# Optimization experiments

Hardware: AMD Instinct MI355X
Metric: run time of the kernel (lower is better)

The kernel has to match this reference:

```python
import jax, jax.numpy as jnp
import numpy as np

B, S, D, H = 2, 2048, 1024, 16
HD = D // H                      # 64
NUM_ROPE_DIMS = 2
NF = HD // (2 * NUM_ROPE_DIMS)   # 16 freqs per rope dim -> total HD//2
FFN_H = 4 * D


def householder_matrix(vs):
    """Product of Householder reflections: Q = prod_i (I - 2 v_i v_i^T / ||v_i||^2)."""
    dim = vs.shape[-1]
    def step(Q, v):
        v = v[:, None]
        Q = Q - (2.0 / (jnp.sum(v * v) + 1e-8)) * (v @ (v.T @ Q))
        return Q, None
    Q, _ = jax.lax.scan(step, jnp.eye(dim, dtype=vs.dtype), vs)
    return Q


def rmsnorm(x):
    # torch.nn.RMSNorm(eps=None) uses dtype eps, no affine
    return x * jax.lax.rsqrt(jnp.mean(x * x, axis=-1, keepdims=True) + jnp.finfo(x.dtype).eps)


def setup_inputs() -> dict:
    key = jax.random.key(0)
    ks = jax.random.split(key, 8)
    x = jax.random.normal(ks[0], (B, S, D), jnp.float32)
    mask = jnp.tril(jnp.ones((S, S), dtype=bool))          # causal block mask
    qkv_w = jax.random.normal(ks[1], (3 * D, D), jnp.float32) * 0.02
    out_w = jax.random.normal(ks[2], (D, D), jnp.float32) * 0.02
    gate_w = jax.random.normal(ks[3], (D, D), jnp.float32) * 0.02
    gate_b = jnp.zeros((D,), jnp.float32)
    w12 = jax.random.normal(ks[4], (2 * FFN_H, D), jnp.float32) * 0.02
    w3 = jax.random.normal(ks[5], (D, FFN_H), jnp.float32) * 0.02
    hh_vs = jax.random.normal(ks[6], (HD // 2, HD), jnp.float32) * 0.02
    inv_freq = 1.0 / (10000.0 ** (jnp.arange(NF, dtype=jnp.float32) / NF))
    pos = jnp.arange(S, dtype=jnp.float32)
    rope_pos = jnp.stack([pos, pos], axis=-1)              # [S, num_rope_dims]
    return dict(x=x, mask=mask, qkv_w=qkv_w, out_w=out_w, gate_w=gate_w,
                gate_b=gate_b, w12=w12, w3=w3, hh_vs=hh_vs,
                inv_freq=inv_freq, rope_pos=rope_pos)


def reference(x, mask, qkv_w, out_w, gate_w, gate_b, w12, w3, hh_vs, inv_freq, rope_pos):
    Bs, Ss, Ds = x.shape
    resid = x
    xn = rmsnorm(x)
    qkv = xn @ qkv_w.T                                      # [B,S,3D]
    q, k, v = jnp.split(qkv, 3, axis=-1)
    q = q.reshape(Bs, Ss, H, HD).transpose(0, 2, 1, 3)      # [B,H,S,HD]
    k = k.reshape(Bs, Ss, H, HD).transpose(0, 2, 1, 3)
    v = v.reshape(Bs, Ss, H, HD).transpose(0, 2, 1, 3)

    # RnRoPE: rotate into canonical basis, apply RoPE, rotate back
    Q = householder_matrix(hh_vs)                           # [HD,HD]
    q = q @ Q.T
    k = k @ Q.T
    # geo_state.scale = 1.0
    full = jnp.einsum('sd,f->sdf', rope_pos, inv_freq).reshape(Ss, -1)  # [S, HD//2]
    half = HD // 2
    full = full[:, :half]
    emb = jnp.concatenate([full, full], axis=-1)            # [S, HD]
    cos, sin = jnp.cos(emb), jnp.sin(emb)

    def rot(t):
        t1, t2 = jnp.split(t, 2, axis=-1)
        return t * cos + jnp.concatenate([-t2, t1], axis=-1) * sin

    q = rot(q) @ Q
    k = rot(k) @ Q

    # block-masked attention (flex_attention default scale = 1/sqrt(HD))
    scores = jnp.einsum('bhsd,bhtd->bhst', q, k) / jnp.sqrt(jnp.asarray(HD, x.dtype))
    scores = jnp.where(mask, scores, -jnp.inf)
    attn = jax.nn.softmax(scores, axis=-1)
    o = jnp.einsum('bhst,bhtd->bhsd', attn, v)
    o = o.transpose(0, 2, 1, 3).reshape(Bs, Ss, Ds)
    o = o @ out_w.T
    gate = jax.nn.sigmoid(o @ gate_w.T + gate_b)
    x = resid + o * gate

    # SwiGLU FFN
    resid2 = x
    xn2 = rmsnorm(x)
    x12 = xn2 @ w12.T
    x1, x2 = jnp.split(x12, 2, axis=-1)
    ffn = (jax.nn.silu(x1) * x2) @ w3.T
    return resid2 + ffn
```

## Files before the change

kernel.cpp:

```cpp
#include <hip/hip_runtime.h>
#include <hip/hip_bf16.h>
#include <math.h>

constexpr int Bc = 2, Sc = 2048, Dc = 1024, Hc = 16, HDc = 64;
constexpr int D3 = 3 * Dc;

typedef __bf16 bf16x8 __attribute__((ext_vector_type(8)));
typedef float f32x4 __attribute__((ext_vector_type(4)));

__device__ __forceinline__ void gll16(const void* g, void* l) {
  __builtin_amdgcn_global_load_lds((const __attribute__((address_space(1))) unsigned int*)g,
                                   (__attribute__((address_space(3))) unsigned int*)l,
                                   16, 0, 0);
}

__device__ __forceinline__ unsigned short f2bf(float v) {
  __hip_bfloat16 h = __float2bfloat16(v);
  return *(unsigned short*)&h;
}
__device__ __forceinline__ float b2f(unsigned short u) {
  unsigned v = ((unsigned)u) << 16;
  return __uint_as_float(v);
}

#define SBAR() asm volatile("s_barrier" ::: "memory")

__global__ __launch_bounds__(256) void f2b_kernel(const float* __restrict__ in,
                                                  unsigned short* __restrict__ out) {
  int i = blockIdx.x * 256 + threadIdx.x;
  float4 v = ((const float4*)in)[i];
  ushort4 o;
  o.x = f2bf(v.x); o.y = f2bf(v.y); o.z = f2bf(v.z); o.w = f2bf(v.w);
  ((ushort4*)out)[i] = o;
}

__global__ __launch_bounds__(256) void w12i_kernel(const float* __restrict__ in,
                                                   unsigned short* __restrict__ out) {
  int r = blockIdx.x;
  int g = r >> 5, u = r & 31;
  int src = ((u < 16) ? 0 : 4096) + g * 16 + (u & 15);
  float4 v = ((const float4*)(in + (size_t)src * 1024))[threadIdx.x];
  ushort4 o;
  o.x = f2bf(v.x); o.y = f2bf(v.y); o.z = f2bf(v.z); o.w = f2bf(v.w);
  ((ushort4*)(out + (size_t)r * 1024))[threadIdx.x] = o;
}

__global__ __launch_bounds__(256) void rmsnorm_bf16_kernel(const float* __restrict__ in,
                                                           unsigned short* __restrict__ out) {
  int row = blockIdx.x;
  const float4* x4 = (const float4*)(in + (size_t)row * Dc);
  float4 v = x4[threadIdx.x];
  float s = v.x * v.x + v.y * v.y + v.z * v.z + v.w * v.w;
#pragma unroll
  for (int off = 1; off < 64; off <<= 1) s += __shfl_xor(s, off);
  __shared__ float wsum[4];
  if ((threadIdx.x & 63) == 0) wsum[threadIdx.x >> 6] = s;
  __syncthreads();
  float tot = wsum[0] + wsum[1] + wsum[2] + wsum[3];
  float r = rsqrtf(tot * (1.0f / Dc) + 1.1920928955078125e-07f);
  ushort4 o;
  o.x = f2bf(v.x * r); o.y = f2bf(v.y * r); o.z = f2bf(v.z * r); o.w = f2bf(v.w * r);
  ((ushort4*)(out + (size_t)row * Dc))[threadIdx.x] = o;
}

__global__ __launch_bounds__(64) void hh_kernel(const float* __restrict__ vs,
                                                float* __restrict__ Qout) {
  __shared__ float Qm[64][65];
  __shared__ float vsh[64];
  int t = threadIdx.x;
  for (int i = 0; i < 64; ++i) Qm[i][t] = (i == t) ? 1.0f : 0.0f;
  for (int it = 0; it < 32; ++it) {
    __syncthreads();
    vsh[t] = vs[it * 64 + t];
    __syncthreads();
    float nv = 0.0f;
    for (int i = 0; i < 64; ++i) nv += vsh[i] * vsh[i];
    float c = 2.0f / (nv + 1e-8f);
    float wj = 0.0f;
    for (int i = 0; i < 64; ++i) wj += vsh[i] * Qm[i][t];
    for (int i = 0; i < 64; ++i) Qm[i][t] -= c * vsh[i] * wj;
  }
  __syncthreads();
  for (int i = 0; i < 64; ++i) Qout[i * 64 + t] = Qm[i][t];
}

__global__ __launch_bounds__(256) void wqk_kernel(const float* __restrict__ W,
                                                  const float* __restrict__ Qm,
                                                  unsigned short* __restrict__ out) {
  int n = blockIdx.x;
  int r = n & 63;
  int base = n & ~63;
  int t = threadIdx.x;
  float a0 = 0, a1 = 0, a2 = 0, a3 = 0;
  const float4* Wp = (const float4*)(W + (size_t)base * 1024) + t;
#pragma unroll 8
  for (int e = 0; e < 64; ++e) {
    float q = Qm[r * 64 + e];
    float4 wv = Wp[(size_t)e * 256];
    a0 += q * wv.x; a1 += q * wv.y; a2 += q * wv.z; a3 += q * wv.w;
  }
  float sc = (n < 1024) ? 0.18033688f : 1.0f;
  ushort4 o;
  o.x = f2bf(a0 * sc); o.y = f2bf(a1 * sc); o.z = f2bf(a2 * sc); o.w = f2bf(a3 * sc);
  ((ushort4*)(out + (size_t)n * 1024))[t] = o;
}

__global__ __launch_bounds__(256) void rtab_kernel(const float* __restrict__ rope_pos,
                                                   const float* __restrict__ inv_freq,
                                                   float2* __restrict__ tab) {
  int id = blockIdx.x * 256 + threadIdx.x;
  int s = id >> 5, d = id & 31;
  float pos = rope_pos[s * 2 + (d >> 4)];
  float emb = pos * inv_freq[d & 15];
  tab[id] = make_float2(cosf(emb), sinf(emb));
}

__global__ __launch_bounds__(256) void rope_kernel(const unsigned short* __restrict__ qkv,
                                                   const float2* __restrict__ tab,
                                                   unsigned short* __restrict__ qb,
                                                   unsigned short* __restrict__ kb) {
  int t = threadIdx.x;
  int gid = blockIdx.x * 64 + (t >> 2);
  int sub = t & 3;
  int h = gid & 15;
  int which = (gid >> 4) & 1;
  int tok = gid >> 5;
  int s = tok & (Sc - 1), b = tok >> 11;
  const unsigned short* src = qkv + (size_t)tok * D3 + which * Dc + h * 64 + sub * 8;
  uint4 lov = *(const uint4*)src;
  uint4 hiv = *(const uint4*)(src + 32);
  const unsigned short* lp = (const unsigned short*)&lov;
  const unsigned short* hp = (const unsigned short*)&hiv;
  unsigned short olo[8], ohi[8];
  const float2* tp = tab + s * 32 + sub * 8;
#pragma unroll
  for (int i = 0; i < 8; ++i) {
    float2 cs = tp[i];
    float lo = b2f(lp[i]), hi = b2f(hp[i]);
    olo[i] = f2bf(lo * cs.x - hi * cs.y);
    ohi[i] = f2bf(hi * cs.x + lo * cs.y);
  }
  unsigned short* dst = (which ? kb : qb) + ((size_t)((b * Hc + h) * Sc + s)) * 64 + sub * 8;
  *(uint4*)dst = *(uint4*)olo;
  *(uint4*)(dst + 32) = *(uint4*)ohi;
}

__global__ __launch_bounds__(256) void vt_kernel(const unsigned short* __restrict__ qkv,
                                                 unsigned short* __restrict__ vtb) {
  __shared__ unsigned short tile[64 * 72];
  int st = blockIdx.x;
  int bh = blockIdx.y;
  int b = bh >> 4, h = bh & 15;
  int t = threadIdx.x;
  int srow = t >> 2, c16 = (t & 3) * 16;
  const unsigned short* src =
      qkv + (size_t)(b * Sc + st * 64 + srow) * D3 + 2 * Dc + h * 64 + c16;
  uint4 a0 = *(const uint4*)src;
  uint4 a1 = *(const uint4*)(src + 8);
  *(uint4*)(tile + srow * 72 + c16) = a0;
  *(uint4*)(tile + srow * 72 + c16 + 8) = a1;
  __syncthreads();
  int d = t >> 2, sch = (t & 3) * 16;
  unsigned short tmp[16];
#pragma unroll
  for (int i = 0; i < 16; ++i) tmp[i] = tile[(sch + i) * 72 + d];
  unsigned short* dst = vtb + ((size_t)(bh * 64 + d)) * Sc + st * 64 + sch;
  *(uint4*)dst = *(uint4*)tmp;
  *(uint4*)(dst + 8) = *(uint4*)(tmp + 8);
}

template <int MODE>
__global__ __launch_bounds__(512, 1) void mgemm8p(const unsigned short* __restrict__ A,
                                                  const unsigned short* __restrict__ B,
                                                  unsigned short* __restrict__ C,
                                                  int M, int N, int K) {
  __shared__ unsigned short lds[65536];
  const int t = threadIdx.x;
  const int lane = t & 63;
  const int wave = t >> 6;
  const int wr = wave >> 2, wc = wave & 3;
  const int l15 = lane & 15, l4 = lane >> 4;
  const int gx = gridDim.x;
  const int nwg = gx * gridDim.y;
  const int id = blockIdx.y * gx + blockIdx.x;
  const int swz = (id & 7) * (nwg >> 3) + (id >> 3);
  const int m0 = (swz / gx) * 256;
  const int n0 = (swz % gx) * 256;
  const int NT = K >> 6;
  const int sko = (((t & 3) ^ ((t >> 3) & 3)) * 8);
  const unsigned short* ag0 = A + (size_t)(m0 + (t >> 2)) * K + sko;
  const unsigned short* ag1 = ag0 + (size_t)128 * K;
  const unsigned short* bg0 = B + (size_t)(n0 + (t >> 2)) * K + sko;
  const unsigned short* bg1 = bg0 + (size_t)128 * K;
  const int t8 = t * 8;
  const int ks = (l4 ^ ((l15 >> 1) & 3)) * 8;
  gll16(ag0, lds + t8);
  gll16(ag1, lds + 4096 + t8);
  gll16(bg0, lds + 32768 + t8);
  gll16(bg1, lds + 32768 + 4096 + t8);
  gll16(ag0 + 32, lds + 8192 + t8);
  gll16(ag1 + 32, lds + 8192 + 4096 + t8);
  gll16(bg0 + 32, lds + 32768 + 8192 + t8);
  gll16(bg1 + 32, lds + 32768 + 8192 + 4096 + t8);
  asm volatile("s_waitcnt vmcnt(4)" ::: "memory");
  SBAR();
  f32x4 acc[8][4] = {};
  for (int kt = 0; kt < NT; ++kt) {
    const int cur = (kt & 1) << 14;
    const int nxt = cur ^ 16384;
    const int kof = ((kt + 1 < NT) ? (kt + 1) : kt) << 6;
    const unsigned short* Ap = lds + cur;
    const unsigned short* Bp = lds + 32768 + cur;
    bf16x8 a[8], b0, b1;
#pragma unroll
    for (int i = 0; i < 8; ++i)
      a[i] = *(const bf16x8*)(Ap + (wr * 128 + i * 16 + l15) * 32 + ks);
    b0 = *(const bf16x8*)(Bp + (wc * 64 + l15) * 32 + ks);
    b1 = *(const bf16x8*)(Bp + (wc * 64 + 16 + l15) * 32 + ks);
    gll16(ag0 + kof, lds + nxt + t8);
    gll16(ag1 + kof, lds + nxt + 4096 + t8);
    SBAR();
    __builtin_amdgcn_s_setprio(1);
#pragma unroll
    for (int i = 0; i < 8; ++i) {
      acc[i][0] = __builtin_amdgcn_mfma_f32_16x16x32_bf16(a[i], b0, acc[i][0], 0, 0, 0);
      acc[i][1] = __builtin_amdgcn_mfma_f32_16x16x32_bf16(a[i], b1, acc[i][1], 0, 0, 0);
    }
    __builtin_amdgcn_s_setprio(0);
    SBAR();
    b0 = *(const bf16x8*)(Bp + (wc * 64 + 32 + l15) * 32 + ks);
    b1 = *(const bf16x8*)(Bp + (wc * 64 + 48 + l15) * 32 + ks);
    gll16(bg0 + kof, lds + 32768 + nxt + t8);
    gll16(bg1 + kof, lds + 32768 + nxt + 4096 + t8);
    asm volatile("s_waitcnt vmcnt(4)" ::: "memory");
    SBAR();
    __builtin_amdgcn_s_setprio(1);
#pragma unroll
    for (int i = 0; i < 8; ++i) {
      acc[i][2] = __builtin_amdgcn_mfma_f32_16x16x32_bf16(a[i], b0, acc[i][2], 0, 0, 0);
      acc[i][3] = __builtin_amdgcn_mfma_f32_16x16x32_bf16(a[i], b1, acc[i][3], 0, 0, 0);
    }
    __builtin_amdgcn_s_setprio(0);
    SBAR();
#pragma unroll
    for (int i = 0; i < 8; ++i)
      a[i] = *(const bf16x8*)(Ap + 8192 + (wr * 128 + i * 16 + l15) * 32 + ks);
    b0 = *(const bf16x8*)(Bp + 8192 + (wc * 64 + l15) * 32 + ks);
    b1 = *(const bf16x8*)(Bp + 8192 + (wc * 64 + 16 + l15) * 32 + ks);
    gll16(ag0 + kof + 32, lds + nxt + 8192 + t8);
    gll16(ag1 + kof + 32, lds + nxt + 8192 + 4096 + t8);
    SBAR();
    __builtin_amdgcn_s_setprio(1);
#pragma unroll
    for (int i = 0; i < 8; ++i) {
      acc[i][0] = __builtin_amdgcn_mfma_f32_16x16x32_bf16(a[i], b0, acc[i][0], 0, 0, 0);
      acc[i][1] = __builtin_amdgcn_mfma_f32_16x16x32_bf16(a[i], b1, acc[i][1], 0, 0, 0);
    }
    __builtin_amdgcn_s_setprio(0);
    SBAR();
    b0 = *(const bf16x8*)(Bp + 8192 + (wc * 64 + 32 + l15) * 32 + ks);
    b1 = *(const bf16x8*)(Bp + 8192 + (wc * 64 + 48 + l15) * 32 + ks);
    gll16(bg0 + kof + 32, lds + 32768 + nxt + 8192 + t8);
    gll16(bg1 + kof + 32, lds + 32768 + nxt + 8192 + 4096 + t8);
    asm volatile("s_waitcnt vmcnt(4)" ::: "memory");
    SBAR();
    __builtin_amdgcn_s_setprio(1);
#pragma unroll
    for (int i = 0; i < 8; ++i) {
      acc[i][2] = __builtin_amdgcn_mfma_f32_16x16x32_bf16(a[i], b0, acc[i][2], 0, 0, 0);
      acc[i][3] = __builtin_amdgcn_mfma_f32_16x16x32_bf16(a[i], b1, acc[i][3], 0, 0, 0);
    }
    __builtin_amdgcn_s_setprio(0);
    SBAR();
  }
  asm volatile("s_waitcnt vmcnt(0)" ::: "memory");
  const int r0 = m0 + wr * 128 + l4 * 4;
  if (MODE == 0) {
    const int c0 = n0 + wc * 64 + l15;
#pragma unroll
    for (int i = 0; i < 8; ++i)
#pragma unroll
      for (int j = 0; j < 4; ++j)
#pragma unroll
        for (int r = 0; r < 4; ++r)
          C[(size_t)(r0 + i * 16 + r) * N + c0 + j * 16] = f2bf(acc[i][j][r]);
  } else {
    const int nc = N >> 1;
    const int c0 = (n0 >> 1) + wc * 32 + l15;
#pragma unroll
    for (int i = 0; i < 8; ++i)
#pragma unroll
      for (int p = 0; p < 2; ++p)
#pragma unroll
        for (int r = 0; r < 4; ++r) {
          float v = acc[i][2 * p][r];
          float sv = v / (1.0f + expf(-v));
          C[(size_t)(r0 + i * 16 + r) * nc + c0 + p * 16] = f2bf(sv * acc[i][2 * p + 1][r]);
        }
  }
}

template <int MODE>
__global__ __launch_bounds__(256, 3) void mgemm64(const unsigned short* __restrict__ A,
                                                  const unsigned short* __restrict__ W,
                                                  const float* __restrict__ R,
                                                  const float* __restrict__ R2,
                                                  const float* __restrict__ bias,
                                                  void* __restrict__ Cout,
                                                  void* __restrict__ Cout2,
                                                  int M, int N, int K) {
  __shared__ unsigned short As[2048];
  __shared__ unsigned short Bs[4096];
  const int t = threadIdx.x;
  const int lane = t & 63;
  const int wave = t >> 6;
  const int wr = wave >> 1, wc = wave & 1;
  const int m0 = blockIdx.y * 64, n0 = blockIdx.x * 128;
  f32x4 acc[2][4] = {};
  const int srow = t >> 2;
  const int sch = (t & 3) * 8;
  const unsigned short* Ag = A + (size_t)(m0 + srow) * K + sch;
  const unsigned short* Wg = W + (size_t)(n0 + srow) * K + sch;
  const size_t rstep = (size_t)64 * K;
  const int frow = lane & 15;
  const int fk = (lane >> 4) * 8;
  for (int k0 = 0; k0 < K; k0 += 32) {
    __syncthreads();
    gll16(Ag + k0, As + t * 8);
    gll16(Wg + k0, Bs + t * 8);
    gll16(Wg + k0 + rstep, Bs + 2048 + t * 8);
    __syncthreads();
    bf16x8 af[2], bq[4];
#pragma unroll
    for (int i = 0; i < 2; ++i)
      af[i] = *(const bf16x8*)(As + (wr * 32 + i * 16 + frow) * 32 + fk);
#pragma unroll
    for (int j = 0; j < 4; ++j)
      bq[j] = *(const bf16x8*)(Bs + (wc * 64 + j * 16 + frow) * 32 + fk);
#pragma unroll
    for (int i = 0; i < 2; ++i)
#pragma unroll
      for (int j = 0; j < 4; ++j)
        acc[i][j] = __builtin_amdgcn_mfma_f32_16x16x32_bf16(af[i], bq[j], acc[i][j], 0, 0, 0);
  }
  const int crow = wr * 32 + (lane >> 4) * 4;
  const int ccol = wc * 64 + (lane & 15);
#pragma unroll
  for (int i = 0; i < 2; ++i) {
#pragma unroll
    for (int j = 0; j < 4; ++j) {
#pragma unroll
      for (int r = 0; r < 4; ++r) {
        int row = m0 + crow + i * 16 + r;
        int col = n0 + ccol + j * 16;
        float v = acc[i][j][r];
        size_t off = (size_t)row * N + col;
        if (MODE == 2) {
          ((float*)Cout)[off] = v + R[off];
        } else if (MODE == 4) {
          ((float*)Cout)[off] = v;
          ((unsigned short*)Cout2)[off] = f2bf(v);
        } else {
          float g = v + bias[col];
          float sg = 1.0f / (1.0f + expf(-g));
          ((float*)Cout)[off] = R[off] + R2[off] * sg;
        }
      }
    }
  }
}

__global__ __launch_bounds__(256) void mattn(const unsigned short* __restrict__ qb,
                                             const unsigned short* __restrict__ kb,
                                             const unsigned short* __restrict__ vtb,
                                             unsigned short* __restrict__ out) {
  __shared__ unsigned short Qs[8192];
  __shared__ unsigned short Ks[2][4096];
  __shared__ unsigned short Vts[2][4096];
  __shared__ unsigned short Ps[4 * 16 * 72];
  const int qt = gridDim.x - 1 - blockIdx.x;
  const int bh = blockIdx.y;
  const int b = bh >> 4, h = bh & 15;
  const int t = threadIdx.x, lane = t & 63, w = t >> 6;
  const int l15 = lane & 15, l4 = lane >> 4;
  const unsigned short* qbase = qb + ((size_t)bh * Sc + qt * 128) * 64;
  const unsigned short* kbase = kb + (size_t)bh * Sc * 64;
  const unsigned short* vbase = vtb + (size_t)bh * 64 * Sc;
#pragma unroll
  for (int i = 0; i < 4; ++i) {
    int idx = t + i * 256;
    int r = idx >> 3;
    int cg = (idx & 7) ^ (r & 7);
    gll16(qbase + (size_t)r * 64 + cg * 8, Qs + idx * 8);
  }
  const int sr = t >> 3;
  const int scg = (t & 7) ^ (sr & 7);
  gll16(kbase + (size_t)sr * 64 + scg * 8, Ks[0] + t * 8);
  gll16(kbase + (size_t)(sr + 32) * 64 + scg * 8, Ks[0] + 2048 + t * 8);
  gll16(vbase + (size_t)sr * Sc + scg * 8, Vts[0] + t * 8);
  gll16(vbase + (size_t)(sr + 32) * Sc + scg * 8, Vts[0] + 2048 + t * 8);
  bf16x8 qf[2][2];
  f32x4 oacc[2][4] = {};
  float lrow[2][4] = {};
  unsigned short* pw = Ps + w * 16 * 72;
  const int ktmax = 2 * qt + 1;
  for (int kt = 0; kt <= ktmax; ++kt) {
    const int cur = kt & 1;
    const int ktn = (kt < ktmax) ? kt + 1 : kt;
    gll16(kbase + (size_t)(ktn * 64 + sr) * 64 + scg * 8, Ks[cur ^ 1] + t * 8);
    gll16(kbase + (size_t)(ktn * 64 + sr + 32) * 64 + scg * 8, Ks[cur ^ 1] + 2048 + t * 8);
    gll16(vbase + (size_t)sr * Sc + ktn * 64 + scg * 8, Vts[cur ^ 1] + t * 8);
    gll16(vbase + (size_t)(sr + 32) * Sc + ktn * 64 + scg * 8, Vts[cur ^ 1] + 2048 + t * 8);
    asm volatile("s_waitcnt vmcnt(4)" ::: "memory");
    SBAR();
    if (kt == 0) {
#pragma unroll
      for (int ch = 0; ch < 2; ++ch) {
        int qrow = ch * 64 + w * 16 + l15;
#pragma unroll
        for (int kc = 0; kc < 2; ++kc)
          qf[ch][kc] = *(const bf16x8*)(Qs + qrow * 64 + (((kc * 4 + l4) ^ (l15 & 7)) * 8));
      }
    }
    const bool actA = (kt <= 2 * qt);
    f32x4 sc[2][4] = {};
#pragma unroll
    for (int kc = 0; kc < 2; ++kc) {
      bf16x8 kf[4];
#pragma unroll
      for (int j = 0; j < 4; ++j)
        kf[j] = *(const bf16x8*)(Ks[cur] + (j * 16 + l15) * 64 + (((kc * 4 + l4) ^ (l15 & 7)) * 8));
      __builtin_amdgcn_s_setprio(1);
      if (actA) {
#pragma unroll
        for (int j = 0; j < 4; ++j)
          sc[0][j] = __builtin_amdgcn_mfma_f32_16x16x32_bf16(qf[0][kc], kf[j], sc[0][j], 0, 0, 0);
      }
#pragma unroll
      for (int j = 0; j < 4; ++j)
        sc[1][j] = __builtin_amdgcn_mfma_f32_16x16x32_bf16(qf[1][kc], kf[j], sc[1][j], 0, 0, 0);
      __builtin_amdgcn_s_setprio(0);
    }
    const int rl = w * 16 + l4 * 4;
    if (kt == 2 * qt) {
#pragma unroll
      for (int j = 0; j < 4; ++j)
#pragma unroll
        for (int r = 0; r < 4; ++r)
          if (j * 16 + l15 > rl + r) sc[0][j][r] = -INFINITY;
    }
    if (kt == ktmax) {
#pragma unroll
      for (int j = 0; j < 4; ++j)
#pragma unroll
        for (int r = 0; r < 4; ++r)
          if (j * 16 + l15 > rl + r) sc[1][j][r] = -INFINITY;
    }
    bf16x8 vf[2][4];
#pragma unroll
    for (int kc = 0; kc < 2; ++kc)
#pragma unroll
      for (int j = 0; j < 4; ++j)
        vf[kc][j] = *(const bf16x8*)(Vts[cur] + (j * 16 + l15) * 64 + (((kc * 4 + l4) ^ (l15 & 7)) * 8));
#pragma unroll
    for (int ch = 0; ch < 2; ++ch) {
      if (ch == 0 && !actA) continue;
#pragma unroll
      for (int j = 0; j < 4; ++j)
#pragma unroll
        for (int r = 0; r < 4; ++r) {
          float p = exp2f(sc[ch][j][r]);
          lrow[ch][r] += p;
          pw[(l4 * 4 + r) * 72 + j * 16 + l15] = f2bf(p);
        }
      __asm__ __volatile__("s_waitcnt lgkmcnt(0)" ::: "memory");
      __builtin_amdgcn_s_setprio(1);
#pragma unroll
      for (int kc = 0; kc < 2; ++kc) {
        bf16x8 pf = *(const bf16x8*)(pw + l15 * 72 + kc * 32 + l4 * 8);
#pragma unroll
        for (int j = 0; j < 4; ++j)
          oacc[ch][j] = __builtin_amdgcn_mfma_f32_16x16x32_bf16(pf, vf[kc][j], oacc[ch][j], 0, 0, 0);
      }
      __builtin_amdgcn_s_setprio(0);
    }
    SBAR();
  }
  asm volatile("s_waitcnt vmcnt(0)" ::: "memory");
#pragma unroll
  for (int ch = 0; ch < 2; ++ch) {
#pragma unroll
    for (int r = 0; r < 4; ++r) {
      float s = lrow[ch][r];
      s += __shfl_xor(s, 1);
      s += __shfl_xor(s, 2);
      s += __shfl_xor(s, 4);
      s += __shfl_xor(s, 8);
      float inv = 1.0f / s;
#pragma unroll
      for (int j = 0; j < 4; ++j) {
        int srow = qt * 128 + ch * 64 + w * 16 + l4 * 4 + r;
        out[((size_t)(b * Sc + srow)) * Dc + h * 64 + j * 16 + l15] =
            f2bf(oacc[ch][j][r] * inv);
      }
    }
  }
}

extern "C" void kernel_launch(void* const* d_in, const int* in_sizes, int n_in,
                              void* d_out, int out_size, void* d_ws, size_t ws_size,
                              hipStream_t stream) {
  const float* x        = (const float*)d_in[0];
  const float* qkv_w    = (const float*)d_in[2];
  const float* out_w    = (const float*)d_in[3];
  const float* gate_w   = (const float*)d_in[4];
  const float* gate_b   = (const float*)d_in[5];
  const float* w12      = (const float*)d_in[6];
  const float* w3       = (const float*)d_in[7];
  const float* hh_vs    = (const float*)d_in[8];
  const float* inv_freq = (const float*)d_in[9];
  const float* rope_pos = (const float*)d_in[10];
  char* ws = (char*)d_ws;
  unsigned short* woutb  = (unsigned short*)(ws + 0);
  float2*         rtab   = (float2*)(ws + 2097152);
  unsigned short* wqkvb  = (unsigned short*)(ws + 4194304);
  unsigned short* attnb  = (unsigned short*)(ws + 4194304);
  float*          xmid   = (float*)(ws + 0);
  unsigned short* slotB  = (unsigned short*)(ws + 16777216);
  float*          oproj  = (float*)(ws + 25165824);
  unsigned short* w12b   = (unsigned short*)(ws + 25165824);
  unsigned short* wgateb = (unsigned short*)(ws + 41943040);
  unsigned short* w3b    = (unsigned short*)(ws + 41943040);
  unsigned short* qkvb   = (unsigned short*)(ws + 58720256);
  unsigned short* hbufb  = (unsigned short*)(ws + 58720256);
  unsigned short* qb     = (unsigned short*)(ws + 83886080);
  unsigned short* oprojb = (unsigned short*)(ws + 83886080);
  unsigned short* kb     = (unsigned short*)(ws + 92274688);
  unsigned short* vtb    = (unsigned short*)(ws + 100663296);
  float*          Qb     = (float*)(ws + 109051904);
  float* outp = (float*)d_out;

  hh_kernel<<<1, 64, 0, stream>>>(hh_vs, Qb);
  rtab_kernel<<<256, 256, 0, stream>>>(rope_pos, inv_freq, rtab);
  wqk_kernel<<<2048, 256, 0, stream>>>(qkv_w, Qb, wqkvb);
  f2b_kernel<<<1024, 256, 0, stream>>>(qkv_w + 2048 * 1024,
                                       wqkvb + 2048 * 1024);
  f2b_kernel<<<1024, 256, 0, stream>>>(out_w, woutb);
  f2b_kernel<<<1024, 256, 0, stream>>>(gate_w, wgateb);
  rmsnorm_bf16_kernel<<<4096, 256, 0, stream>>>(x, slotB);
  mgemm8p<0><<<dim3(12, 16), 512, 0, stream>>>(slotB, wqkvb, qkvb, 4096, 3072, 1024);
  rope_kernel<<<2048, 256, 0, stream>>>(qkvb, rtab, qb, kb);
  vt_kernel<<<dim3(32, 32), 256, 0, stream>>>(qkvb, vtb);
  mattn<<<dim3(16, 32), 256, 0, stream>>>(qb, kb, vtb, attnb);
  mgemm64<4><<<dim3(8, 64), 256, 0, stream>>>(attnb, woutb, nullptr, nullptr, nullptr,
                                              oproj, oprojb, 4096, 1024, 1024);
  mgemm64<5><<<dim3(8, 64), 256, 0, stream>>>(oprojb, wgateb, x, oproj, gate_b,
                                              xmid, nullptr, 4096, 1024, 1024);
  w12i_kernel<<<8192, 256, 0, stream>>>(w12, w12b);
  f2b_kernel<<<4096, 256, 0, stream>>>(w3, w3b);
  rmsnorm_bf16_kernel<<<4096, 256, 0, stream>>>(xmid, slotB);
  mgemm8p<1><<<dim3(32, 16), 512, 0, stream>>>(slotB, w12b, hbufb, 4096, 8192, 1024);
  mgemm64<2><<<dim3(8, 64), 256, 0, stream>>>(hbufb, w3b, xmid, nullptr, nullptr,
                                              outp, nullptr, 4096, 1024, 4096);
}
```

Before: 569.4 us.

## Double-buffer mgemm64 LDS tiles and single-buffer V in attention for occupancy

```diff
diff --git a/kernel.cpp b/kernel.cpp
--- a/kernel.cpp
+++ b/kernel.cpp
@@ -294,7 +294,7 @@
 #pragma unroll
         for (int r = 0; r < 4; ++r) {
           float v = acc[i][2 * p][r];
-          float sv = v / (1.0f + expf(-v));
+          float sv = v / (1.0f + __expf(-v));
           C[(size_t)(r0 + i * 16 + r) * nc + c0 + p * 16] = f2bf(sv * acc[i][2 * p + 1][r]);
         }
   }
@@ -309,8 +309,8 @@
                                                   void* __restrict__ Cout,
                                                   void* __restrict__ Cout2,
                                                   int M, int N, int K) {
-  __shared__ unsigned short As[2048];
-  __shared__ unsigned short Bs[4096];
+  __shared__ unsigned short As[2][2048];
+  __shared__ unsigned short Bs[2][4096];
   const int t = threadIdx.x;
   const int lane = t & 63;
   const int wave = t >> 6;
@@ -324,25 +324,34 @@
   const size_t rstep = (size_t)64 * K;
   const int frow = lane & 15;
   const int fk = (lane >> 4) * 8;
+  gll16(Ag, As[0] + t * 8);
+  gll16(Wg, Bs[0] + t * 8);
+  gll16(Wg + rstep, Bs[0] + 2048 + t * 8);
   for (int k0 = 0; k0 < K; k0 += 32) {
-    __syncthreads();
-    gll16(Ag + k0, As + t * 8);
-    gll16(Wg + k0, Bs + t * 8);
-    gll16(Wg + k0 + rstep, Bs + 2048 + t * 8);
-    __syncthreads();
+    const int cur = (k0 >> 5) & 1;
+    const int kn = (k0 + 32 < K) ? (k0 + 32) : k0;
+    gll16(Ag + kn, As[cur ^ 1] + t * 8);
+    gll16(Wg + kn, Bs[cur ^ 1] + t * 8);
+    gll16(Wg + kn + rstep, Bs[cur ^ 1] + 2048 + t * 8);
+    asm volatile("s_waitcnt vmcnt(3)" ::: "memory");
+    SBAR();
     bf16x8 af[2], bq[4];
 #pragma unroll
     for (int i = 0; i < 2; ++i)
-      af[i] = *(const bf16x8*)(As + (wr * 32 + i * 16 + frow) * 32 + fk);
+      af[i] = *(const bf16x8*)(As[cur] + (wr * 32 + i * 16 + frow) * 32 + fk);
 #pragma unroll
     for (int j = 0; j < 4; ++j)
-      bq[j] = *(const bf16x8*)(Bs + (wc * 64 + j * 16 + frow) * 32 + fk);
+      bq[j] = *(const bf16x8*)(Bs[cur] + (wc * 64 + j * 16 + frow) * 32 + fk);
+    __builtin_amdgcn_s_setprio(1);
 #pragma unroll
     for (int i = 0; i < 2; ++i)
 #pragma unroll
       for (int j = 0; j < 4; ++j)
         acc[i][j] = __builtin_amdgcn_mfma_f32_16x16x32_bf16(af[i], bq[j], acc[i][j], 0, 0, 0);
-  }
+    __builtin_amdgcn_s_setprio(0);
+    SBAR();
+  }
+  asm volatile("s_waitcnt vmcnt(0)" ::: "memory");
   const int crow = wr * 32 + (lane >> 4) * 4;
   const int ccol = wc * 64 + (lane & 15);
 #pragma unroll
@@ -362,7 +371,7 @@
           ((unsigned short*)Cout2)[off] = f2bf(v);
         } else {
           float g = v + bias[col];
-          float sg = 1.0f / (1.0f + expf(-g));
+          float sg = 1.0f / (1.0f + __expf(-g));
           ((float*)Cout)[off] = R[off] + R2[off] * sg;
         }
       }
@@ -370,13 +379,13 @@
   }
 }
 
-__global__ __launch_bounds__(256) void mattn(const unsigned short* __restrict__ qb,
-                                             const unsigned short* __restrict__ kb,
-                                             const unsigned short* __restrict__ vtb,
-                                             unsigned short* __restrict__ out) {
+__global__ __launch_bounds__(256, 3) void mattn(const unsigned short* __restrict__ qb,
+                                                const unsigned short* __restrict__ kb,
+                                                const unsigned short* __restrict__ vtb,
+                                                unsigned short* __restrict__ out) {
   __shared__ unsigned short Qs[8192];
   __shared__ unsigned short Ks[2][4096];
-  __shared__ unsigned short Vts[2][4096];
+  __shared__ unsigned short Vts[4096];
   __shared__ unsigned short Ps[4 * 16 * 72];
   const int qt = gridDim.x - 1 - blockIdx.x;
   const int bh = blockIdx.y;
@@ -395,10 +404,10 @@
   }
   const int sr = t >> 3;
   const int scg = (t & 7) ^ (sr & 7);
+  gll16(vbase + (size_t)sr * Sc + scg * 8, Vts + t * 8);
+  gll16(vbase + (size_t)(sr + 32) * Sc + scg * 8, Vts + 2048 + t * 8);
   gll16(kbase + (size_t)sr * 64 + scg * 8, Ks[0] + t * 8);
   gll16(kbase + (size_t)(sr + 32) * 64 + scg * 8, Ks[0] + 2048 + t * 8);
-  gll16(vbase + (size_t)sr * Sc + scg * 8, Vts[0] + t * 8);
-  gll16(vbase + (size_t)(sr + 32) * Sc + scg * 8, Vts[0] + 2048 + t * 8);
   bf16x8 qf[2][2];
   f32x4 oacc[2][4] = {};
   float lrow[2][4] = {};
@@ -406,12 +415,18 @@
   const int ktmax = 2 * qt + 1;
   for (int kt = 0; kt <= ktmax; ++kt) {
     const int cur = kt & 1;
+    if (kt > 0) {
+      gll16(vbase + (size_t)sr * Sc + kt * 64 + scg * 8, Vts + t * 8);
+      gll16(vbase + (size_t)(sr + 32) * Sc + kt * 64 + scg * 8, Vts + 2048 + t * 8);
+    }
     const int ktn = (kt < ktmax) ? kt + 1 : kt;
     gll16(kbase + (size_t)(ktn * 64 + sr) * 64 + scg * 8, Ks[cur ^ 1] + t * 8);
     gll16(kbase + (size_t)(ktn * 64 + sr + 32) * 64 + scg * 8, Ks[cur ^ 1] + 2048 + t * 8);
-    gll16(vbase + (size_t)sr * Sc + ktn * 64 + scg * 8, Vts[cur ^ 1] + t * 8);
-    gll16(vbase + (size_t)(sr + 32) * Sc + ktn * 64 + scg * 8, Vts[cur ^ 1] + 2048 + t * 8);
-    asm volatile("s_waitcnt vmcnt(4)" ::: "memory");
+    if (kt == 0) {
+      asm volatile("s_waitcnt vmcnt(2)" ::: "memory");
+    } else {
+      asm volatile("s_waitcnt vmcnt(4)" ::: "memory");
+    }
     SBAR();
     if (kt == 0) {
 #pragma unroll
@@ -456,12 +471,14 @@
         for (int r = 0; r < 4; ++r)
           if (j * 16 + l15 > rl + r) sc[1][j][r] = -INFINITY;
     }
+    asm volatile("s_waitcnt vmcnt(2)" ::: "memory");
+    SBAR();
     bf16x8 vf[2][4];
 #pragma unroll
     for (int kc = 0; kc < 2; ++kc)
 #pragma unroll
       for (int j = 0; j < 4; ++j)
-        vf[kc][j] = *(const bf16x8*)(Vts[cur] + (j * 16 + l15) * 64 + (((kc * 4 + l4) ^ (l15 & 7)) * 8));
+        vf[kc][j] = *(const bf16x8*)(Vts + (j * 16 + l15) * 64 + (((kc * 4 + l4) ^ (l15 & 7)) * 8));
 #pragma unroll
     for (int ch = 0; ch < 2; ++ch) {
       if (ch == 0 && !actA) continue;
```

After: 557.4 us. 2.1% less time.
